# Performance work log

Measured on AMD Instinct MI355X. Metric: run time of the kernel, lower is better.

Reference implementation:

```python
import jax, jax.numpy as jnp
import numpy as np

RAY_DIR = jnp.array([0.4395064455, 0.617598629942, 0.652231566745], dtype=jnp.float32)
TOL = 1e-7
CONTACT_THRESH = 25.0   # opt.contact_thresh
COLLISION_THRESH = 25.0  # opt.collision_thresh
BIG = 1e10


def mesh_contains(points, triangles, tri_valid):
    """Moller-Trumbore ray casting (fixed ray dir), parity test.
    points [B,P,3], triangles [B,T,3,3], tri_valid [B,T] -> exterior [B,P] bool."""
    v0, v1, v2 = triangles[:, :, 0, :], triangles[:, :, 1, :], triangles[:, :, 2, :]
    e1 = v1 - v0
    e2 = v2 - v0
    pvec = jnp.cross(jnp.broadcast_to(RAY_DIR, e2.shape), e2)          # [B,T,3]
    dets = jnp.sum(e1 * pvec, -1)                                      # [B,T]
    parallel = jnp.abs(dets) < TOL
    invdet = 1.0 / (dets + 0.1 * TOL)
    tvec = points[:, None, :, :] - v0[:, :, None, :]                   # [B,T,P,3]
    u = jnp.sum(tvec * pvec[:, :, None, :], -1) * invdet[:, :, None]   # [B,T,P]
    qvec = jnp.cross(tvec, e1[:, :, None, :])                          # [B,T,P,3]
    v = jnp.sum(qvec * RAY_DIR, -1) * invdet[:, :, None]
    t = jnp.sum(e2[:, :, None, :] * qvec, -1) * invdet[:, :, None]
    inter = (u > 0) & (u < 1) & (v > 0) & (u + v < 1) & (t > TOL)
    inter = inter & (~parallel & tri_valid)[:, :, None]
    n_hits = jnp.sum(inter.astype(jnp.int32), axis=1)                  # [B,P]
    return (n_hits % 2) == 0


def masked_mean_loss(vals, mask):
    m = mask.astype(vals.dtype)
    tot = m.sum()
    loss = jnp.where(tot > 0, (m * vals).sum() / jnp.maximum(tot, 1.0), 0.0)
    row = m.sum(1)
    losses = jnp.where(row > 0, (m * vals).sum(1) / jnp.maximum(row, 1.0), 0.0)
    return loss, losses


def setup_inputs() -> dict:
    key = jax.random.key(0)
    ks = jax.random.split(key, 6)
    B, Nh, Fh, No, Fo = 8, 778, 1538, 2000, 4000
    hand_verts = jax.random.normal(ks[0], (B, Nh, 3), dtype=jnp.float32)
    hand_faces = jax.random.randint(ks[1], (B, Fh, 3), 0, Nh, dtype=jnp.int32)
    obj_verts = jax.random.normal(ks[2], (B, No, 3), dtype=jnp.float32)
    obj_faces = jax.random.randint(ks[3], (B, Fo, 3), 0, 1200, dtype=jnp.int32)
    obj_vert_splits = 1200 + jax.random.randint(ks[4], (B,), 0, No - 1200 + 1, dtype=jnp.int32)
    obj_face_splits = 2400 + jax.random.randint(ks[5], (B,), 0, Fo - 2400 + 1, dtype=jnp.int32)
    return {"hand_verts": hand_verts, "hand_faces": hand_faces,
            "obj_verts": obj_verts, "obj_faces": obj_faces,
            "obj_vert_splits": obj_vert_splits, "obj_face_splits": obj_face_splits}


def reference(hand_verts, hand_faces, obj_verts, obj_faces, obj_vert_splits, obj_face_splits):
    B, Nh, _ = hand_verts.shape
    No = obj_verts.shape[1]
    Fo = obj_faces.shape[1]
    sg = jax.lax.stop_gradient

    # gather triangles (batched)
    hand_tri = jax.vmap(lambda v, f: v[f])(hand_verts, hand_faces)     # [B,Fh,3,3]
    obj_tri = jax.vmap(lambda v, f: v[f])(obj_verts, obj_faces)        # [B,Fo,3,3]

    face_valid = jnp.arange(Fo)[None, :] < obj_face_splits[:, None]    # [B,Fo]
    vert_valid = jnp.arange(No)[None, :] < obj_vert_splits[:, None]    # [B,No]

    # containment tests run on detached geometry (as in original)
    hand_tri_valid = jnp.ones(hand_tri.shape[:2], dtype=bool)
    exterior_obj = mesh_contains(sg(obj_verts), sg(hand_tri), hand_tri_valid)   # [B,No]
    exterior_hand = mesh_contains(sg(hand_verts), sg(obj_tri), face_valid)      # [B,Nh]

    penetr_o_mask = (~exterior_obj) & vert_valid
    penetr_h_mask = ~exterior_hand

    # ragged squared pairwise distances (bmm form of original), padded cols -> BIG
    rx = jnp.sum(hand_verts * hand_verts, -1)                          # [B,Nh]
    ry = jnp.sum(obj_verts * obj_verts, -1)                            # [B,No]
    zz = jnp.einsum('bnd,bmd->bnm', hand_verts, obj_verts)             # [B,Nh,No]
    dists = rx[:, :, None] + ry[:, None, :] - 2.0 * zz
    dists = jnp.where(vert_valid[:, None, :], dists, BIG)

    minoh_idxs = jnp.argmin(dists, axis=1)                             # [B,No]
    minho_idxs = jnp.argmin(dists, axis=2)                             # [B,Nh]

    results_close = jnp.take_along_axis(obj_verts, minho_idxs[:, :, None], axis=1)    # [B,Nh,3]
    results_o_close = jnp.take_along_axis(hand_verts, minoh_idxs[:, :, None], axis=1)  # [B,No,3]

    # contact_target == 'all'
    anchor_dists = jnp.sqrt(jnp.sum((results_close - hand_verts) ** 2, -1))    # [B,Nh]
    anchor_o_dist = jnp.sqrt(jnp.sum((results_o_close - obj_verts) ** 2, -1))  # [B,No]

    # contact_mode == 'dist_tanh' -> below_dist all ones
    contact_vals = CONTACT_THRESH * jnp.tanh(anchor_dists / CONTACT_THRESH)
    # collision_mode == 'dist_tanh'
    collision_vals = COLLISION_THRESH * jnp.tanh(anchor_dists / COLLISION_THRESH)
    collision_o_vals = COLLISION_THRESH * jnp.tanh(anchor_o_dist / COLLISION_THRESH)
    collision_o_vals = jnp.where(vert_valid, collision_o_vals, 0.0)

    # contact_zones == 'all'
    missed_mask = exterior_hand

    missed_loss, missed_losses = masked_mean_loss(contact_vals, missed_mask)
    penetr_h_loss, penetr_h_losses = masked_mean_loss(collision_vals, penetr_h_mask)
    penetr_o_loss, penetr_o_losses = masked_mean_loss(collision_o_vals, penetr_o_mask)
    penetr_loss = penetr_h_loss + penetr_o_loss
    penetr_losses = penetr_h_losses + penetr_o_losses

    return missed_loss, penetr_loss, missed_losses, penetr_losses
```

## Files before the change

kernel.cpp:

```cpp
#include <hip/hip_runtime.h>


#define RX 0.4395064455f
#define RY 0.617598629942f
#define RZ 0.652231566745f

#define MAXCHUNK_F4 512
#define PTS_PER_BLK 512

struct Params {
    const float* hand_verts; const int* hand_faces;
    const float* obj_verts;  const int* obj_faces;
    const int* ovsplit; const int* ofsplit;
    int* hitsA;
    int* hitsB;
    float* anchor_h; float* anchor_o;
    float* partials;
    unsigned int* done;
    float* out;
    int B, Nh, Fh, No, Fo;
    int pbA, CA, chunkA, blocksA;
    int pbB, CB, chunkB, blocksB;
};

__device__ __forceinline__ void tri_pre_one(const float* __restrict__ vb,
                                            const int* __restrict__ f,
                                            float4* o) {
#pragma clang fp contract(off)
    int i0 = f[0], i1 = f[1], i2 = f[2];
    float v0x = vb[i0*3+0], v0y = vb[i0*3+1], v0z = vb[i0*3+2];
    float v1x = vb[i1*3+0], v1y = vb[i1*3+1], v1z = vb[i1*3+2];
    float v2x = vb[i2*3+0], v2y = vb[i2*3+1], v2z = vb[i2*3+2];
    float e1x = v1x - v0x, e1y = v1y - v0y, e1z = v1z - v0z;
    float e2x = v2x - v0x, e2y = v2y - v0y, e2z = v2z - v0z;
    float px = RY*e2z - RZ*e2y;
    float py = RZ*e2x - RX*e2z;
    float pz = RX*e2y - RY*e2x;
    float det = (e1x*px + e1y*py) + e1z*pz;
    float invdet = 1.0f / (det + 1e-8f);
    if (fabsf(det) < 1e-7f) invdet = 0.0f;
    o[0] = make_float4(v0x, v0y, v0z, invdet);
    o[1] = make_float4(e1x, e1y, e1z, 0.0f);
    o[2] = make_float4(e2x, e2y, e2z, 0.0f);
    o[3] = make_float4(px,  py,  pz,  0.0f);
}

__device__ __forceinline__ int mt_test(float qx, float qy, float qz,
                                       const float4& f0, const float4& f1,
                                       const float4& f2, const float4& f3) {
#pragma clang fp contract(off)
    float tvx = qx - f0.x, tvy = qy - f0.y, tvz = qz - f0.z;
    float u  = ((tvx*f3.x + tvy*f3.y) + tvz*f3.z) * f0.w;
    float qvx = tvy*f1.z - tvz*f1.y;
    float qvy = tvz*f1.x - tvx*f1.z;
    float qvz = tvx*f1.y - tvy*f1.x;
    float v  = ((qvx*RX + qvy*RY) + qvz*RZ) * f0.w;
    float tt = ((f2.x*qvx + f2.y*qvy) + f2.z*qvz) * f0.w;
    bool hit = (u > 0.0f) && (u < 1.0f) && (v > 0.0f) &&
               ((u + v) < 1.0f) && (tt > 1e-7f);
    return hit ? 1 : 0;
}

__device__ __forceinline__ void raycast_vb(const Params& p, int vbid, int tid,
                                           float4* s_tri) {
#pragma clang fp contract(off)
    const float* pts; const float* tverts; const int* tfaces; int* slots;
    int P, T, Nv, c, pb, b, chunk, tlim, plim;
    if (vbid < p.blocksA) {
        int per_b = p.pbA * p.CA;
        b  = vbid / per_b;
        int r = vbid - b * per_b;
        c  = r / p.pbA;
        pb = r - c * p.pbA;
        pts = p.obj_verts; tverts = p.hand_verts; tfaces = p.hand_faces;
        slots = p.hitsA;
        P = p.No; T = p.Fh; Nv = p.Nh; chunk = p.chunkA;
        tlim = p.Fh; plim = min(p.No, p.ovsplit[b]);
    } else {
        int j = vbid - p.blocksA;
        int per_b = p.pbB * p.CB;
        b  = j / per_b;
        int r = j - b * per_b;
        c  = r / p.pbB;
        pb = r - c * p.pbB;
        pts = p.hand_verts; tverts = p.obj_verts; tfaces = p.obj_faces;
        slots = p.hitsB;
        P = p.Nh; T = p.Fo; Nv = p.No; chunk = p.chunkB;
        tlim = min(p.Fo, p.ofsplit[b]); plim = p.Nh;
    }

    int tStart = c * chunk;
    if (tStart >= tlim) return;
    if (pb * PTS_PER_BLK >= plim) return;
    int nTri = min(tStart + chunk, tlim) - tStart;

    if (tid < nTri) {
        int t = tStart + tid;
        tri_pre_one(tverts + (size_t)b * Nv * 3,
                    tfaces + ((size_t)b * T + t) * 3,
                    s_tri + (size_t)tid * 4);
    }

    int p1 = pb * PTS_PER_BLK + tid;
    int p2 = p1 + 256;
    bool act1 = p1 < plim, act2 = p2 < plim;
    float q1x = 0.f, q1y = 0.f, q1z = 0.f;
    float q2x = 0.f, q2y = 0.f, q2z = 0.f;
    if (act1) {
        const float* q = pts + ((size_t)b * P + p1) * 3;
        q1x = q[0]; q1y = q[1]; q1z = q[2];
    }
    if (act2) {
        const float* q = pts + ((size_t)b * P + p2) * 3;
        q2x = q[0]; q2y = q[1]; q2z = q[2];
    }
    __syncthreads();

    if (!act1) return;
    int cnt1 = 0, cnt2 = 0;
    if (__any(act2)) {
        for (int i = 0; i < nTri; ++i) {
            const float4 f0 = s_tri[(i<<2)+0];
            const float4 f1 = s_tri[(i<<2)+1];
            const float4 f2 = s_tri[(i<<2)+2];
            const float4 f3 = s_tri[(i<<2)+3];
            cnt1 += mt_test(q1x, q1y, q1z, f0, f1, f2, f3);
            cnt2 += mt_test(q2x, q2y, q2z, f0, f1, f2, f3);
        }
    } else {
        for (int i = 0; i < nTri; ++i) {
            const float4 f0 = s_tri[(i<<2)+0];
            const float4 f1 = s_tri[(i<<2)+1];
            const float4 f2 = s_tri[(i<<2)+2];
            const float4 f3 = s_tri[(i<<2)+3];
            cnt1 += mt_test(q1x, q1y, q1z, f0, f1, f2, f3);
        }
    }
    int* base = slots + ((size_t)(c * p.B + b)) * P;
    base[p1] = cnt1;
    if (act2) base[p2] = cnt2;
}

__device__ __forceinline__ void min_one(const Params& p, int w, int lane) {
#pragma clang fp contract(off)
    int nHand = p.B * p.Nh;
    const float* refv; const float* loopv; int loopN; float* outp;
    if (w < nHand) {
        int b = w / p.Nh;
        int n = w - b * p.Nh;
        refv  = p.hand_verts + ((size_t)b * p.Nh + n) * 3;
        loopv = p.obj_verts + (size_t)b * p.No * 3;
        loopN = p.ovsplit[b];
        outp  = p.anchor_h + (size_t)b * p.Nh + n;
    } else {
        int j = w - nHand;
        int b = j / p.No;
        int m = j - b * p.No;
        if (m >= p.ovsplit[b]) return;
        refv  = p.obj_verts + ((size_t)b * p.No + m) * 3;
        loopv = p.hand_verts + (size_t)b * p.Nh * 3;
        loopN = p.Nh;
        outp  = p.anchor_o + (size_t)b * p.No + m;
    }
    float hx = refv[0], hy = refv[1], hz = refv[2];
    float rx = (hx*hx + hy*hy) + hz*hz;
    unsigned long long best = ~0ull;
    for (int m = lane; m < loopN; m += 64) {
        float ox = loopv[m*3+0], oy = loopv[m*3+1], oz = loopv[m*3+2];
        float ry = (ox*ox + oy*oy) + oz*oz;
        float zz = (hx*ox + hy*oy) + hz*oz;
        float d = (rx + ry) - 2.0f * zz;
        unsigned long long e = ((unsigned long long)__float_as_uint(d) << 32) | (unsigned)m;
        if (e < best) best = e;
    }
    for (int off = 32; off > 0; off >>= 1) {
        unsigned long long o = __shfl_xor(best, off, 64);
        if (o < best) best = o;
    }
    if (lane == 0) {
        int idx = (best == ~0ull) ? 0 : (int)(best & 0xffffffffu);
        const float* cv = loopv + (size_t)idx * 3;
        float dx = cv[0] - hx, dy = cv[1] - hy, dz = cv[2] - hz;
        *outp = sqrtf((dx*dx + dy*dy) + dz*dz);
    }
}

__global__ __launch_bounds__(256) void mega(Params p) {
    __shared__ float4 s_tri[MAXCHUNK_F4];
    const int tid = threadIdx.x;
    const int bid = blockIdx.x;
    if (bid == 0 && tid == 0) *p.done = 0u;
    const int nRay = p.blocksA + p.blocksB;
    if (bid < nRay) {
        raycast_vb(p, bid, tid, s_tri);
    } else {
        int w = (bid - nRay) * 4 + (tid >> 6);
        if (w < p.B * (p.Nh + p.No)) min_one(p, w, tid & 63);
    }
}

__global__ __launch_bounds__(64) void reduce_fin(Params p) {
    const int r    = blockIdx.x;
    const int b    = r >> 4;
    const int wv   = r & 15;
    const int lane = threadIdx.x;
    const int vt   = wv * 64 + lane;
    float s0=0.f,s1=0.f,s2=0.f,s3=0.f,s4=0.f,s5=0.f;

    int tlimB = min(p.Fo, p.ofsplit[b]);
    int nCB = (tlimB + p.chunkB - 1) / p.chunkB;
    for (int n = vt; n < p.Nh; n += 1024) {
        int par = 0;
        for (int c = 0; c < nCB; ++c)
            par += p.hitsB[((size_t)(c * p.B + b)) * p.Nh + n];
        bool ext = (par & 1) == 0;
        float val = 25.0f * tanhf(p.anchor_h[(size_t)b*p.Nh + n] / 25.0f);
        if (ext) { s0 += val; s1 += 1.0f; } else { s2 += val; s3 += 1.0f; }
    }
    int split = p.ovsplit[b];
    for (int m = vt; m < split; m += 1024) {
        int par = 0;
        for (int c = 0; c < p.CA; ++c)
            par += p.hitsA[((size_t)(c * p.B + b)) * p.No + m];
        if (par & 1) {
            s4 += 25.0f * tanhf(p.anchor_o[(size_t)b*p.No + m] / 25.0f);
            s5 += 1.0f;
        }
    }
    for (int off = 32; off > 0; off >>= 1) {
        s0 += __shfl_xor(s0, off, 64);
        s1 += __shfl_xor(s1, off, 64);
        s2 += __shfl_xor(s2, off, 64);
        s3 += __shfl_xor(s3, off, 64);
        s4 += __shfl_xor(s4, off, 64);
        s5 += __shfl_xor(s5, off, 64);
    }

    __shared__ bool s_last;
    if (lane == 0) {
        float* q = p.partials + ((size_t)(b * 16 + wv)) * 6;
        q[0]=s0; q[1]=s1; q[2]=s2; q[3]=s3; q[4]=s4; q[5]=s5;
        __threadfence();
        unsigned int old = atomicAdd(p.done, 1u);
        s_last = (old == (unsigned int)(gridDim.x - 1));
    }
    __syncthreads();
    if (!s_last) return;
    __threadfence();

    __shared__ float s_red[16][6];
    if (lane < p.B && lane < 16) {
        int bb = lane;
        float t0=0.f,t1=0.f,t2=0.f,t3=0.f,t4=0.f,t5=0.f;
        for (int w2 = 0; w2 < 16; ++w2) {
            const float* q = p.partials + ((size_t)(bb * 16 + w2)) * 6;
            t0 += q[0]; t1 += q[1]; t2 += q[2];
            t3 += q[3]; t4 += q[4]; t5 += q[5];
        }
        p.out[2 + bb]  = (t1 > 0.f) ? t0 / fmaxf(t1, 1.f) : 0.f;
        float ph       = (t3 > 0.f) ? t2 / fmaxf(t3, 1.f) : 0.f;
        float po       = (t5 > 0.f) ? t4 / fmaxf(t5, 1.f) : 0.f;
        p.out[10 + bb] = ph + po;
        s_red[bb][0]=t0; s_red[bb][1]=t1; s_red[bb][2]=t2;
        s_red[bb][3]=t3; s_red[bb][4]=t4; s_red[bb][5]=t5;
    }
    __syncthreads();
    if (lane == 0) {
        float sm=0.f,cm=0.f,sph=0.f,cph=0.f,spo=0.f,cpo=0.f;
        for (int bb = 0; bb < p.B; ++bb) {
            sm  += s_red[bb][0]; cm  += s_red[bb][1]; sph += s_red[bb][2];
            cph += s_red[bb][3]; spo += s_red[bb][4]; cpo += s_red[bb][5];
        }
        float missed = (cm  > 0.f) ? sm  / fmaxf(cm , 1.f) : 0.f;
        float ph     = (cph > 0.f) ? sph / fmaxf(cph, 1.f) : 0.f;
        float po     = (cpo > 0.f) ? spo / fmaxf(cpo, 1.f) : 0.f;
        p.out[0] = missed;
        p.out[1] = ph + po;
    }
}

extern "C" void kernel_launch(void* const* d_in, const int* in_sizes, int n_in,
                              void* d_out, int out_size, void* d_ws, size_t ws_size,
                              hipStream_t stream) {
    Params p;
    p.hand_verts = (const float*)d_in[0];
    p.hand_faces = (const int*)d_in[1];
    p.obj_verts  = (const float*)d_in[2];
    p.obj_faces  = (const int*)d_in[3];
    p.ovsplit    = (const int*)d_in[4];
    p.ofsplit    = (const int*)d_in[5];
    p.out        = (float*)d_out;

    p.B  = in_sizes[4];
    p.Nh = in_sizes[0] / (3 * p.B);
    p.Fh = in_sizes[1] / (3 * p.B);
    p.No = in_sizes[2] / (3 * p.B);
    p.Fo = in_sizes[3] / (3 * p.B);

    p.CA = 16; p.CB = 32;
    p.chunkA = (p.Fh + p.CA - 1) / p.CA;
    p.chunkB = (p.Fo + p.CB - 1) / p.CB;
    p.pbA = (p.No + PTS_PER_BLK - 1) / PTS_PER_BLK;
    p.pbB = (p.Nh + PTS_PER_BLK - 1) / PTS_PER_BLK;
    p.blocksA = p.pbA * p.CA * p.B;
    p.blocksB = p.pbB * p.CB * p.B;

    char* ws = (char*)d_ws;
    size_t off = 0;
    auto alloc = [&](size_t bytes) -> void* {
        void* q = ws + off;
        off = (off + bytes + 255) & ~(size_t)255;
        return q;
    };
    p.hitsA    = (int*)   alloc((size_t)p.CA * p.B * p.No * sizeof(int));
    p.hitsB    = (int*)   alloc((size_t)p.CB * p.B * p.Nh * sizeof(int));
    p.anchor_h = (float*) alloc((size_t)p.B * p.Nh * sizeof(float));
    p.anchor_o = (float*) alloc((size_t)p.B * p.No * sizeof(float));
    p.partials = (float*) alloc((size_t)p.B * 16 * 6 * sizeof(float));
    p.done     = (unsigned int*)alloc(sizeof(unsigned int));

    int totalMin   = p.B * (p.Nh + p.No);
    int nMinBlocks = (totalMin + 3) / 4;
    int grid = p.blocksA + p.blocksB + nMinBlocks;

    mega<<<grid, 256, 0, stream>>>(p);
    reduce_fin<<<p.B * 16, 64, 0, stream>>>(p);
}
```

Measured before the change: 132.2 us.

## Fuse final reduction into main kernel via spin-wait and widen raycast point blocks

The separate reduction kernel becomes extra blocks at the end of the main grid. Those blocks spin on a global completion counter until all raycast and nearest-vertex blocks have finished, which removes a second kernel launch. Each raycast thread now tests four points instead of two (1024 points per block), which halves the triangle preprocessing repeated across blocks. The risks are spin-wait deadlock if the reduction blocks become resident before the work blocks, the added hipMemsetAsync call, and higher register pressure from four points per thread.

```diff
diff --git a/kernel.cpp b/kernel.cpp
--- a/kernel.cpp
+++ b/kernel.cpp
@@ -6,7 +6,7 @@
 #define RZ 0.652231566745f
 
 #define MAXCHUNK_F4 512
-#define PTS_PER_BLK 512
+#define PTS_PER_BLK 1024
 
 struct Params {
     const float* hand_verts; const int* hand_faces;
@@ -21,6 +21,7 @@
     int B, Nh, Fh, No, Fo;
     int pbA, CA, chunkA, blocksA;
     int pbB, CB, chunkB, blocksB;
+    int nMinBlk, nVB;
 };
 
 __device__ __forceinline__ void tri_pre_one(const float* __restrict__ vb,
@@ -102,30 +103,47 @@
     }
 
     int p1 = pb * PTS_PER_BLK + tid;
-    int p2 = p1 + 256;
-    bool act1 = p1 < plim, act2 = p2 < plim;
-    float q1x = 0.f, q1y = 0.f, q1z = 0.f;
-    float q2x = 0.f, q2y = 0.f, q2z = 0.f;
-    if (act1) {
-        const float* q = pts + ((size_t)b * P + p1) * 3;
-        q1x = q[0]; q1y = q[1]; q1z = q[2];
-    }
-    if (act2) {
-        const float* q = pts + ((size_t)b * P + p2) * 3;
-        q2x = q[0]; q2y = q[1]; q2z = q[2];
-    }
+    int p2 = p1 + 256, p3 = p1 + 512, p4 = p1 + 768;
+    bool act1 = p1 < plim, act2 = p2 < plim, act3 = p3 < plim, act4 = p4 < plim;
+    float q1x=0.f,q1y=0.f,q1z=0.f, q2x=0.f,q2y=0.f,q2z=0.f;
+    float q3x=0.f,q3y=0.f,q3z=0.f, q4x=0.f,q4y=0.f,q4z=0.f;
+    if (act1) { const float* q = pts + ((size_t)b*P + p1)*3; q1x=q[0]; q1y=q[1]; q1z=q[2]; }
+    if (act2) { const float* q = pts + ((size_t)b*P + p2)*3; q2x=q[0]; q2y=q[1]; q2z=q[2]; }
+    if (act3) { const float* q = pts + ((size_t)b*P + p3)*3; q3x=q[0]; q3y=q[1]; q3z=q[2]; }
+    if (act4) { const float* q = pts + ((size_t)b*P + p4)*3; q4x=q[0]; q4y=q[1]; q4z=q[2]; }
     __syncthreads();
 
     if (!act1) return;
-    int cnt1 = 0, cnt2 = 0;
-    if (__any(act2)) {
+    int c1=0, c2=0, c3=0, c4=0;
+    if (__any(act4)) {
         for (int i = 0; i < nTri; ++i) {
             const float4 f0 = s_tri[(i<<2)+0];
             const float4 f1 = s_tri[(i<<2)+1];
             const float4 f2 = s_tri[(i<<2)+2];
             const float4 f3 = s_tri[(i<<2)+3];
-            cnt1 += mt_test(q1x, q1y, q1z, f0, f1, f2, f3);
-            cnt2 += mt_test(q2x, q2y, q2z, f0, f1, f2, f3);
+            c1 += mt_test(q1x,q1y,q1z, f0,f1,f2,f3);
+            c2 += mt_test(q2x,q2y,q2z, f0,f1,f2,f3);
+            c3 += mt_test(q3x,q3y,q3z, f0,f1,f2,f3);
+            c4 += mt_test(q4x,q4y,q4z, f0,f1,f2,f3);
+        }
+    } else if (__any(act3)) {
+        for (int i = 0; i < nTri; ++i) {
+            const float4 f0 = s_tri[(i<<2)+0];
+            const float4 f1 = s_tri[(i<<2)+1];
+            const float4 f2 = s_tri[(i<<2)+2];
+            const float4 f3 = s_tri[(i<<2)+3];
+            c1 += mt_test(q1x,q1y,q1z, f0,f1,f2,f3);
+            c2 += mt_test(q2x,q2y,q2z, f0,f1,f2,f3);
+            c3 += mt_test(q3x,q3y,q3z, f0,f1,f2,f3);
+        }
+    } else if (__any(act2)) {
+        for (int i = 0; i < nTri; ++i) {
+            const float4 f0 = s_tri[(i<<2)+0];
+            const float4 f1 = s_tri[(i<<2)+1];
+            const float4 f2 = s_tri[(i<<2)+2];
+            const float4 f3 = s_tri[(i<<2)+3];
+            c1 += mt_test(q1x,q1y,q1z, f0,f1,f2,f3);
+            c2 += mt_test(q2x,q2y,q2z, f0,f1,f2,f3);
         }
     } else {
         for (int i = 0; i < nTri; ++i) {
@@ -133,12 +151,14 @@
             const float4 f1 = s_tri[(i<<2)+1];
             const float4 f2 = s_tri[(i<<2)+2];
             const float4 f3 = s_tri[(i<<2)+3];
-            cnt1 += mt_test(q1x, q1y, q1z, f0, f1, f2, f3);
+            c1 += mt_test(q1x,q1y,q1z, f0,f1,f2,f3);
         }
     }
     int* base = slots + ((size_t)(c * p.B + b)) * P;
-    base[p1] = cnt1;
-    if (act2) base[p2] = cnt2;
+    base[p1] = c1;
+    if (act2) base[p2] = c2;
+    if (act3) base[p3] = c3;
+    if (act4) base[p4] = c4;
 }
 
 __device__ __forceinline__ void min_one(const Params& p, int w, int lane) {
@@ -185,26 +205,10 @@
     }
 }
 
-__global__ __launch_bounds__(256) void mega(Params p) {
-    __shared__ float4 s_tri[MAXCHUNK_F4];
-    const int tid = threadIdx.x;
-    const int bid = blockIdx.x;
-    if (bid == 0 && tid == 0) *p.done = 0u;
-    const int nRay = p.blocksA + p.blocksB;
-    if (bid < nRay) {
-        raycast_vb(p, bid, tid, s_tri);
-    } else {
-        int w = (bid - nRay) * 4 + (tid >> 6);
-        if (w < p.B * (p.Nh + p.No)) min_one(p, w, tid & 63);
-    }
-}
-
-__global__ __launch_bounds__(64) void reduce_fin(Params p) {
-    const int r    = blockIdx.x;
-    const int b    = r >> 4;
-    const int wv   = r & 15;
-    const int lane = threadIdx.x;
-    const int vt   = wv * 64 + lane;
+__device__ void reduce_unit(const Params& p, int unit, int lane) {
+    const int b  = unit >> 4;
+    const int wv = unit & 15;
+    const int vt = wv * 64 + lane;
     float s0=0.f,s1=0.f,s2=0.f,s3=0.f,s4=0.f,s5=0.f;
 
     int tlimB = min(p.Fo, p.ofsplit[b]);
@@ -236,22 +240,20 @@
         s5 += __shfl_xor(s5, off, 64);
     }
 
-    __shared__ bool s_last;
+    unsigned int old = 0u;
     if (lane == 0) {
         float* q = p.partials + ((size_t)(b * 16 + wv)) * 6;
         q[0]=s0; q[1]=s1; q[2]=s2; q[3]=s3; q[4]=s4; q[5]=s5;
         __threadfence();
-        unsigned int old = atomicAdd(p.done, 1u);
-        s_last = (old == (unsigned int)(gridDim.x - 1));
-    }
-    __syncthreads();
-    if (!s_last) return;
+        old = atomicAdd(&p.done[1], 1u);
+    }
+    old = __shfl(old, 0);
+    if (old != (unsigned int)(p.B * 16 - 1)) return;
     __threadfence();
 
-    __shared__ float s_red[16][6];
-    if (lane < p.B && lane < 16) {
+    float t0=0.f,t1=0.f,t2=0.f,t3=0.f,t4=0.f,t5=0.f;
+    if (lane < p.B) {
         int bb = lane;
-        float t0=0.f,t1=0.f,t2=0.f,t3=0.f,t4=0.f,t5=0.f;
         for (int w2 = 0; w2 < 16; ++w2) {
             const float* q = p.partials + ((size_t)(bb * 16 + w2)) * 6;
             t0 += q[0]; t1 += q[1]; t2 += q[2];
@@ -261,21 +263,51 @@
         float ph       = (t3 > 0.f) ? t2 / fmaxf(t3, 1.f) : 0.f;
         float po       = (t5 > 0.f) ? t4 / fmaxf(t5, 1.f) : 0.f;
         p.out[10 + bb] = ph + po;
-        s_red[bb][0]=t0; s_red[bb][1]=t1; s_red[bb][2]=t2;
-        s_red[bb][3]=t3; s_red[bb][4]=t4; s_red[bb][5]=t5;
-    }
-    __syncthreads();
+    }
+    float sm=0.f,cm=0.f,sph=0.f,cph=0.f,spo=0.f,cpo=0.f;
+    for (int bb = 0; bb < p.B; ++bb) {
+        sm  += __shfl(t0, bb); cm  += __shfl(t1, bb); sph += __shfl(t2, bb);
+        cph += __shfl(t3, bb); spo += __shfl(t4, bb); cpo += __shfl(t5, bb);
+    }
     if (lane == 0) {
-        float sm=0.f,cm=0.f,sph=0.f,cph=0.f,spo=0.f,cpo=0.f;
-        for (int bb = 0; bb < p.B; ++bb) {
-            sm  += s_red[bb][0]; cm  += s_red[bb][1]; sph += s_red[bb][2];
-            cph += s_red[bb][3]; spo += s_red[bb][4]; cpo += s_red[bb][5];
-        }
         float missed = (cm  > 0.f) ? sm  / fmaxf(cm , 1.f) : 0.f;
         float ph     = (cph > 0.f) ? sph / fmaxf(cph, 1.f) : 0.f;
         float po     = (cpo > 0.f) ? spo / fmaxf(cpo, 1.f) : 0.f;
         p.out[0] = missed;
         p.out[1] = ph + po;
+    }
+}
+
+__global__ __launch_bounds__(256) void mega(Params p) {
+    __shared__ float4 s_tri[MAXCHUNK_F4];
+    const int tid = threadIdx.x;
+    const int bid = blockIdx.x;
+    const int nRay = p.blocksA + p.blocksB;
+
+    if (bid < p.nVB) {
+        if (bid < nRay) {
+            raycast_vb(p, bid, tid, s_tri);
+        } else {
+            int w = (bid - nRay) * 4 + (tid >> 6);
+            if (w < p.B * (p.Nh + p.No)) min_one(p, w, tid & 63);
+        }
+        __syncthreads();
+        if (tid == 0)
+            __hip_atomic_fetch_add(&p.done[0], 1u, __ATOMIC_RELEASE,
+                                   __HIP_MEMORY_SCOPE_AGENT);
+    } else {
+        int unit = (bid - p.nVB) * 4 + (tid >> 6);
+        int lane = tid & 63;
+        if (unit < p.B * 16) {
+            if (lane == 0) {
+                while (__hip_atomic_load(&p.done[0], __ATOMIC_ACQUIRE,
+                                         __HIP_MEMORY_SCOPE_AGENT)
+                       < (unsigned int)p.nVB)
+                    __builtin_amdgcn_s_sleep(32);
+            }
+            __threadfence();
+            reduce_unit(p, unit, lane);
+        }
     }
 }
 
@@ -304,6 +336,12 @@
     p.pbB = (p.Nh + PTS_PER_BLK - 1) / PTS_PER_BLK;
     p.blocksA = p.pbA * p.CA * p.B;
     p.blocksB = p.pbB * p.CB * p.B;
+
+    int totalMin = p.B * (p.Nh + p.No);
+    p.nMinBlk = (totalMin + 3) / 4;
+    p.nVB = p.blocksA + p.blocksB + p.nMinBlk;
+    int nRed = (p.B * 16 + 3) / 4;
+    int grid = p.nVB + nRed;
 
     char* ws = (char*)d_ws;
     size_t off = 0;
@@ -317,12 +355,8 @@
     p.anchor_h = (float*) alloc((size_t)p.B * p.Nh * sizeof(float));
     p.anchor_o = (float*) alloc((size_t)p.B * p.No * sizeof(float));
     p.partials = (float*) alloc((size_t)p.B * 16 * 6 * sizeof(float));
-    p.done     = (unsigned int*)alloc(sizeof(unsigned int));
-
-    int totalMin   = p.B * (p.Nh + p.No);
-    int nMinBlocks = (totalMin + 3) / 4;
-    int grid = p.blocksA + p.blocksB + nMinBlocks;
-
+    p.done     = (unsigned int*)alloc(2 * sizeof(unsigned int));
+
+    hipMemsetAsync((void*)p.done, 0, 2 * sizeof(unsigned int), stream);
     mega<<<grid, 256, 0, stream>>>(p);
-    reduce_fin<<<p.B * 16, 64, 0, stream>>>(p);
-}
+}
```

Result: slower. 211.1 us (+59.6%).
